# Kernel tuning notes

Hardware: AMD Instinct MI355X
Metric: run time of the kernel (lower is better)

Reference implementation:

```python
import jax, jax.numpy as jnp
import numpy as np

N_NODES = 100000
N_EDGES = 1000000
D_IN = 64
D_OUT = 64
K_HOPS = 3


def setup_inputs() -> dict:
    key = jax.random.key(0)
    k1, k2, k3 = jax.random.split(key, 3)
    x = jax.random.normal(k1, (N_NODES, D_IN), dtype=jnp.float32)
    edge_index = jax.random.randint(k2, (2, N_EDGES), 0, N_NODES, dtype=jnp.int64)
    # Linear layer params (PyG Linear: y = x @ W.T + b)
    W = jax.random.normal(k3, (D_OUT, D_IN), dtype=jnp.float32) * (1.0 / np.sqrt(D_IN))
    b = jnp.zeros((D_OUT,), dtype=jnp.float32)
    return {"x": x, "edge_index": edge_index, "W": W, "b": b}


def reference(x, edge_index, W, b):
    # SGConv: x' = (D^{-1/2} (A + I) D^{-1/2})^K x, then Linear.
    N = x.shape[0]
    src, dst = edge_index[0], edge_index[1]
    loop = jnp.arange(N, dtype=edge_index.dtype)
    src = jnp.concatenate([src, loop])  # add self loops
    dst = jnp.concatenate([dst, loop])
    ones = jnp.ones(src.shape[0], dtype=x.dtype)
    deg = jax.ops.segment_sum(ones, dst, num_segments=N)  # in-degree incl. self loop
    dinv = jnp.where(deg > 0, jax.lax.rsqrt(deg), jnp.zeros_like(deg))
    norm = dinv[src] * dinv[dst]  # [E+N]
    for _ in range(K_HOPS):
        # out[dst] += norm * x[src]
        x = jax.ops.segment_sum(norm[:, None] * x[src], dst, num_segments=N)
    return x @ W.T + b
```

## Files before the change

kernel.cpp:

```cpp
#include <hip/hip_runtime.h>

#define NN 100000
#define NE 1000000
#define D  64
#define CAP 32
#define OVF_CAP 16384

#define FILL_EPT 8
#define FILL_CHUNK (256 * FILL_EPT)
#define FILL_NCHUNK ((NE + FILL_CHUNK - 1) / FILL_CHUNK)
#define PART_SZ 12500

__device__ __forceinline__ unsigned bf16rne(float f) {
    unsigned h = __float_as_uint(f);
    return (h + 0x7fffu + ((h >> 16) & 1u)) >> 16;
}
__device__ __forceinline__ uint2 pack4(float4 v) {
    uint2 o;
    o.x = bf16rne(v.x) | (bf16rne(v.y) << 16);
    o.y = bf16rne(v.z) | (bf16rne(v.w) << 16);
    return o;
}
__device__ __forceinline__ float4 unpack4(uint2 u) {
    float4 f;
    f.x = __uint_as_float(u.x << 16);
    f.y = __uint_as_float(u.x & 0xffff0000u);
    f.z = __uint_as_float(u.y << 16);
    f.w = __uint_as_float(u.y & 0xffff0000u);
    return f;
}

__global__ __launch_bounds__(256) void k_fill_bucket(const int* __restrict__ src,
                                                     const int* __restrict__ dst,
                                                     int* __restrict__ cnt,
                                                     int* __restrict__ bucket,
                                                     int* __restrict__ ovf_n,
                                                     int2* __restrict__ ovf) {
    const int part = blockIdx.x & 7;
    const int lo = part * PART_SZ, hi = lo + PART_SZ;
    const int base = (blockIdx.x >> 3) * FILL_CHUNK + threadIdx.x;
    #pragma unroll
    for (int it = 0; it < FILL_EPT; ++it) {
        int e = base + it * 256;
        if (e < NE) {
            int d = __builtin_nontemporal_load(&dst[e]);
            if (d >= lo && d < hi) {
                int s = __builtin_nontemporal_load(&src[e]);
                int c = atomicAdd(&cnt[d], 1);
                if (c < CAP) {
                    bucket[(size_t)d * CAP + c] = s;
                } else {
                    int i = atomicAdd(ovf_n, 1);
                    if (i < OVF_CAP) ovf[i] = make_int2(s, d);
                }
            }
        }
    }
}

__global__ void k_cvt(const float2* __restrict__ x2, unsigned* __restrict__ xb,
                      const int* __restrict__ cnt, float* __restrict__ dinv) {
    int i = blockIdx.x * blockDim.x + threadIdx.x;
    unsigned long long v = __builtin_nontemporal_load((const unsigned long long*)&x2[i]);
    float vx = __uint_as_float((unsigned)(v & 0xffffffffu));
    float vy = __uint_as_float((unsigned)(v >> 32));
    xb[i] = bf16rne(vx) | (bf16rne(vy) << 16);
    if (i < NN) dinv[i] = rsqrtf((float)(cnt[i] + 1));
}


__global__ __launch_bounds__(256) void k_gather_bf16(const uint2* __restrict__ in2,
                                                     const int* __restrict__ cnt,
                                                     const int* __restrict__ bucket,
                                                     const float* __restrict__ dinv,
                                                     const int* __restrict__ ovf_n,
                                                     const int2* __restrict__ ovf,
                                                     uint2* __restrict__ out2) {
    const int tid = threadIdx.x;
    const int l = tid & 15;
    const int n = blockIdx.x * 16 + (tid >> 4);

    const int deg = min(cnt[n], CAP);
    const float dn = dinv[n];

    float4 a0 = unpack4(in2[(size_t)n * 16 + l]);
    a0.x *= dn; a0.y *= dn; a0.z *= dn; a0.w *= dn;
    float4 a1 = make_float4(0.f, 0.f, 0.f, 0.f);
    float4 a2 = make_float4(0.f, 0.f, 0.f, 0.f);
    float4 a3 = make_float4(0.f, 0.f, 0.f, 0.f);

    if (deg > 0) {
        int   iA = (l < deg) ? l : 0;
        int   sA = bucket[(size_t)n * CAP + iA];
        float wA = dinv[sA];
        const int kmax = deg < 16 ? deg : 16;
        int k = 0;
        for (; k + 3 < kmax; k += 4) {
            int   s0 = __shfl(sA, k + 0, 16);
            int   s1 = __shfl(sA, k + 1, 16);
            int   s2 = __shfl(sA, k + 2, 16);
            int   s3 = __shfl(sA, k + 3, 16);
            float w0 = __shfl(wA, k + 0, 16);
            float w1 = __shfl(wA, k + 1, 16);
            float w2 = __shfl(wA, k + 2, 16);
            float w3 = __shfl(wA, k + 3, 16);
            float4 r0 = unpack4(in2[(size_t)s0 * 16 + l]);
            float4 r1 = unpack4(in2[(size_t)s1 * 16 + l]);
            float4 r2 = unpack4(in2[(size_t)s2 * 16 + l]);
            float4 r3 = unpack4(in2[(size_t)s3 * 16 + l]);
            a0.x = fmaf(w0, r0.x, a0.x); a0.y = fmaf(w0, r0.y, a0.y);
            a0.z = fmaf(w0, r0.z, a0.z); a0.w = fmaf(w0, r0.w, a0.w);
            a1.x = fmaf(w1, r1.x, a1.x); a1.y = fmaf(w1, r1.y, a1.y);
            a1.z = fmaf(w1, r1.z, a1.z); a1.w = fmaf(w1, r1.w, a1.w);
            a2.x = fmaf(w2, r2.x, a2.x); a2.y = fmaf(w2, r2.y, a2.y);
            a2.z = fmaf(w2, r2.z, a2.z); a2.w = fmaf(w2, r2.w, a2.w);
            a3.x = fmaf(w3, r3.x, a3.x); a3.y = fmaf(w3, r3.y, a3.y);
            a3.z = fmaf(w3, r3.z, a3.z); a3.w = fmaf(w3, r3.w, a3.w);
        }
        for (; k < kmax; ++k) {
            int   s0 = __shfl(sA, k, 16);
            float w0 = __shfl(wA, k, 16);
            float4 r0 = unpack4(in2[(size_t)s0 * 16 + l]);
            a0.x = fmaf(w0, r0.x, a0.x); a0.y = fmaf(w0, r0.y, a0.y);
            a0.z = fmaf(w0, r0.z, a0.z); a0.w = fmaf(w0, r0.w, a0.w);
        }
        if (deg > 16) {
            int   iB = (16 + l < deg) ? (16 + l) : 0;
            int   sB = bucket[(size_t)n * CAP + iB];
            float wB = dinv[sB];
            const int k2max = deg - 16;
            int k2 = 0;
            for (; k2 + 1 < k2max; k2 += 2) {
                int   s0 = __shfl(sB, k2 + 0, 16);
                int   s1 = __shfl(sB, k2 + 1, 16);
                float w0 = __shfl(wB, k2 + 0, 16);
                float w1 = __shfl(wB, k2 + 1, 16);
                float4 r0 = unpack4(in2[(size_t)s0 * 16 + l]);
                float4 r1 = unpack4(in2[(size_t)s1 * 16 + l]);
                a1.x = fmaf(w0, r0.x, a1.x); a1.y = fmaf(w0, r0.y, a1.y);
                a1.z = fmaf(w0, r0.z, a1.z); a1.w = fmaf(w0, r0.w, a1.w);
                a2.x = fmaf(w1, r1.x, a2.x); a2.y = fmaf(w1, r1.y, a2.y);
                a2.z = fmaf(w1, r1.z, a2.z); a2.w = fmaf(w1, r1.w, a2.w);
            }
            if (k2 < k2max) {
                int   s0 = __shfl(sB, k2, 16);
                float w0 = __shfl(wB, k2, 16);
                float4 r0 = unpack4(in2[(size_t)s0 * 16 + l]);
                a3.x = fmaf(w0, r0.x, a3.x); a3.y = fmaf(w0, r0.y, a3.y);
                a3.z = fmaf(w0, r0.z, a3.z); a3.w = fmaf(w0, r0.w, a3.w);
            }
        }
    }

    int m = *ovf_n;
    if (m > 0) {
        if (m > OVF_CAP) m = OVF_CAP;
        for (int i = 0; i < m; ++i) {
            int2 p = ovf[i];
            if (p.y == n) {
                float w = dinv[p.x];
                float4 r = unpack4(in2[(size_t)p.x * 16 + l]);
                a0.x = fmaf(w, r.x, a0.x); a0.y = fmaf(w, r.y, a0.y);
                a0.z = fmaf(w, r.z, a0.z); a0.w = fmaf(w, r.w, a0.w);
            }
        }
    }

    float4 r;
    r.x = dn * ((a0.x + a1.x) + (a2.x + a3.x));
    r.y = dn * ((a0.y + a1.y) + (a2.y + a3.y));
    r.z = dn * ((a0.z + a1.z) + (a2.z + a3.z));
    r.w = dn * ((a0.w + a1.w) + (a2.w + a3.w));
    out2[(size_t)n * 16 + l] = pack4(r);
}

__global__ __launch_bounds__(256) void k_linear_reg(const unsigned short* __restrict__ inb,
                                                    const float* __restrict__ W,
                                                    const float* __restrict__ bias,
                                                    float* __restrict__ out) {
    const int lane = threadIdx.x & 63;
    const int wid  = (blockIdx.x * blockDim.x + threadIdx.x) >> 6;
    const int nw   = (gridDim.x * blockDim.x) >> 6;

    float w[64];
    const float4* W4 = (const float4*)W;
    #pragma unroll
    for (int i = 0; i < 16; ++i) {
        float4 q = W4[lane * 16 + i];
        w[4 * i + 0] = q.x; w[4 * i + 1] = q.y;
        w[4 * i + 2] = q.z; w[4 * i + 3] = q.w;
    }
    const float bo = bias[lane];

    for (int n = wid; n < NN; n += nw) {
        unsigned short rh = __builtin_nontemporal_load(&inb[(size_t)n * 64 + lane]);
        int rli = (int)((unsigned)rh << 16);
        float y0 = bo, y1 = 0.f;
        #pragma unroll
        for (int i = 0; i < 64; i += 2) {
            y0 = fmaf(__int_as_float(__builtin_amdgcn_readlane(rli, i)),     w[i],     y0);
            y1 = fmaf(__int_as_float(__builtin_amdgcn_readlane(rli, i + 1)), w[i + 1], y1);
        }
        __builtin_nontemporal_store(y0 + y1, &out[(size_t)n * 64 + lane]);
    }
}


__global__ void k_init_deg(float* __restrict__ deg) {
    int n = blockIdx.x * blockDim.x + threadIdx.x;
    if (n < NN) deg[n] = 1.0f;
}
__global__ void k_count_deg(const int* __restrict__ dst, float* __restrict__ deg) {
    int e = blockIdx.x * blockDim.x + threadIdx.x;
    if (e < NE) atomicAdd(&deg[dst[e]], 1.0f);
}
__global__ void k_dinv_f(float* __restrict__ deg) {
    int n = blockIdx.x * blockDim.x + threadIdx.x;
    if (n < NN) deg[n] = rsqrtf(deg[n]);
}
__global__ void k_prop_init(const float* __restrict__ in, const float* __restrict__ dinv,
                            float* __restrict__ out) {
    int i = blockIdx.x * blockDim.x + threadIdx.x;
    if (i < NN * D) {
        int n = i >> 6;
        float di = dinv[n];
        out[i] = di * di * in[i];
    }
}
__global__ __launch_bounds__(256) void k_prop_edges(const float* __restrict__ in,
                                                    const int* __restrict__ src,
                                                    const int* __restrict__ dst,
                                                    const float* __restrict__ dinv,
                                                    float* __restrict__ out) {
    int t = blockIdx.x * blockDim.x + threadIdx.x;
    int e = t >> 6, f = t & 63;
    if (e < NE) {
        int s = src[e], d = dst[e];
        float w = dinv[s] * dinv[d];
        atomicAdd(&out[d * D + f], w * in[s * D + f]);
    }
}
__global__ __launch_bounds__(256) void k_linear(const float* __restrict__ in,
                                                const float* __restrict__ W,
                                                const float* __restrict__ bias,
                                                float* __restrict__ out) {
    __shared__ float Wt[64 * 65];
    __shared__ float rows[4][64];
    const int tid = threadIdx.x;
    for (int m = tid; m < 64 * 64; m += 256) {
        int o = m >> 6, i = m & 63;
        Wt[i * 65 + o] = W[m];
    }
    __syncthreads();
    const int wave = tid >> 6, lane = tid & 63;
    const float bo = bias[lane];
    for (int base = blockIdx.x * 4; base < NN; base += gridDim.x * 4) {
        int n = base + wave;
        if (n < NN) {
            rows[wave][lane] = in[n * D + lane];
            float acc = bo;
            #pragma unroll
            for (int i = 0; i < 64; ++i)
                acc = fmaf(rows[wave][i], Wt[i * 65 + lane], acc);
            out[n * D + lane] = acc;
        }
    }
}


extern "C" void kernel_launch(void* const* d_in, const int* in_sizes, int n_in,
                              void* d_out, int out_size, void* d_ws, size_t ws_size,
                              hipStream_t stream) {
    const float* x   = (const float*)d_in[0];
    const int*   ei  = (const int*)d_in[1];
    const float* W   = (const float*)d_in[2];
    const float* b   = (const float*)d_in[3];
    float* out = (float*)d_out;

    const int* src = ei;
    const int* dst = ei + NE;

    char* ws = (char*)d_ws;
    size_t off = 0;
    auto take = [&](size_t bytes) -> char* {
        char* p = ws + off;
        off = (off + bytes + 255) & ~(size_t)255;
        return p;
    };

    int*      cnt    = (int*)take((size_t)NN * 4);
    float*    dinv   = (float*)take((size_t)NN * 4);
    int*      ovf_n  = (int*)take(256);
    int2*     ovf    = (int2*)take((size_t)OVF_CAP * 8);
    unsigned* P      = (unsigned*)take((size_t)NN * 32 * 4);
    unsigned* Q      = (unsigned*)take((size_t)NN * 32 * 4);
    int*      bucket = (int*)take((size_t)NN * CAP * 4);
    float*    buf    = (float*)P;
    const bool use_bucket = (off <= ws_size);

    const int B = 256;
    const int gridE1 = (NE + B - 1) / B;
    const int gridN1 = (NN + B - 1) / B;
    const int gridNW = NN / 16;

    if (use_bucket) {
        hipMemsetAsync(cnt, 0, (size_t)NN * 4, stream);
        hipMemsetAsync(ovf_n, 0, 4, stream);
        k_fill_bucket<<<FILL_NCHUNK * 8, B, 0, stream>>>(src, dst, cnt, bucket, ovf_n, ovf);
        k_cvt<<<12500, B, 0, stream>>>((const float2*)x, P, cnt, dinv);

        k_gather_bf16<<<gridNW, B, 0, stream>>>((const uint2*)P, cnt, bucket, dinv, ovf_n, ovf, (uint2*)Q);
        k_gather_bf16<<<gridNW, B, 0, stream>>>((const uint2*)Q, cnt, bucket, dinv, ovf_n, ovf, (uint2*)P);
        k_gather_bf16<<<gridNW, B, 0, stream>>>((const uint2*)P, cnt, bucket, dinv, ovf_n, ovf, (uint2*)Q);
        k_linear_reg<<<1024, B, 0, stream>>>((const unsigned short*)Q, W, b, out);
    } else {
        const int gridF = (NN * D + B - 1) / B;
        const int gridEW = (NE * 64) / B;
        k_init_deg <<<gridN1, B, 0, stream>>>(dinv);
        k_count_deg<<<gridE1, B, 0, stream>>>(dst, dinv);
        k_dinv_f   <<<gridN1, B, 0, stream>>>(dinv);
        k_prop_init <<<gridF, B, 0, stream>>>(x, dinv, buf);
        k_prop_edges<<<gridEW, B, 0, stream>>>(x, src, dst, dinv, buf);
        k_prop_init <<<gridF, B, 0, stream>>>(buf, dinv, out);
        k_prop_edges<<<gridEW, B, 0, stream>>>(buf, src, dst, dinv, out);
        k_prop_init <<<gridF, B, 0, stream>>>(out, dinv, buf);
        k_prop_edges<<<gridEW, B, 0, stream>>>(out, src, dst, dinv, buf);
        k_linear<<<NN / 4, B, 0, stream>>>(buf, W, b, out);
    }
}
```

Measured before the change: 173.7 us.

## Fold memsets into convert kernel, stage bucket fill via LDS, recompute dinv inline

Zeroing of the degree counters and overflow counter moves into the bf16 conversion kernel, which now runs before bucket fill, so the two memset launches go away. The separate dinv array is dropped and each gather recomputes rsqrt(cnt+1) from the counts. The fill kernel first collects its selected edges into a shared-memory list and only then does the global atomics. This trims launches and dinv traffic at the cost of extra cnt loads and rsqrt work in every gather pass, plus an extra barrier and LDS staging in the fill kernel.

```diff
diff --git a/kernel.cpp b/kernel.cpp
--- a/kernel.cpp
+++ b/kernel.cpp
@@ -10,6 +10,7 @@
 #define FILL_CHUNK (256 * FILL_EPT)
 #define FILL_NCHUNK ((NE + FILL_CHUNK - 1) / FILL_CHUNK)
 #define PART_SZ 12500
+#define SELCAP 512
 
 __device__ __forceinline__ unsigned bf16rne(float f) {
     unsigned h = __float_as_uint(f);
@@ -30,49 +31,63 @@
     return f;
 }
 
+__global__ void k_cvt(const float2* __restrict__ x2, unsigned* __restrict__ xb,
+                      int* __restrict__ cnt, int* __restrict__ ovf_n) {
+    int i = blockIdx.x * blockDim.x + threadIdx.x;
+    unsigned long long v = __builtin_nontemporal_load((const unsigned long long*)&x2[i]);
+    float vx = __uint_as_float((unsigned)(v & 0xffffffffu));
+    float vy = __uint_as_float((unsigned)(v >> 32));
+    xb[i] = bf16rne(vx) | (bf16rne(vy) << 16);
+    if (i < NN) cnt[i] = 0;
+    if (i == 0) *ovf_n = 0;
+}
+
 __global__ __launch_bounds__(256) void k_fill_bucket(const int* __restrict__ src,
                                                      const int* __restrict__ dst,
                                                      int* __restrict__ cnt,
                                                      int* __restrict__ bucket,
                                                      int* __restrict__ ovf_n,
                                                      int2* __restrict__ ovf) {
+    __shared__ int nsel;
+    __shared__ int2 sel[SELCAP];
     const int part = blockIdx.x & 7;
     const int lo = part * PART_SZ, hi = lo + PART_SZ;
     const int base = (blockIdx.x >> 3) * FILL_CHUNK + threadIdx.x;
+
+    if (threadIdx.x == 0) nsel = 0;
+    __syncthreads();
+
     #pragma unroll
     for (int it = 0; it < FILL_EPT; ++it) {
         int e = base + it * 256;
-        if (e < NE) {
-            int d = __builtin_nontemporal_load(&dst[e]);
-            if (d >= lo && d < hi) {
-                int s = __builtin_nontemporal_load(&src[e]);
+        int d = (e < NE) ? __builtin_nontemporal_load(&dst[e]) : -1;
+        if (d >= lo && d < hi) {
+            int s = __builtin_nontemporal_load(&src[e]);
+            int slot = atomicAdd(&nsel, 1);
+            if (slot < SELCAP) {
+                sel[slot] = make_int2(s, d);
+            } else {
                 int c = atomicAdd(&cnt[d], 1);
-                if (c < CAP) {
-                    bucket[(size_t)d * CAP + c] = s;
-                } else {
-                    int i = atomicAdd(ovf_n, 1);
-                    if (i < OVF_CAP) ovf[i] = make_int2(s, d);
-                }
+                if (c < CAP) bucket[(size_t)d * CAP + c] = s;
+                else { int i = atomicAdd(ovf_n, 1); if (i < OVF_CAP) ovf[i] = make_int2(s, d); }
             }
         }
     }
-}
-
-__global__ void k_cvt(const float2* __restrict__ x2, unsigned* __restrict__ xb,
-                      const int* __restrict__ cnt, float* __restrict__ dinv) {
-    int i = blockIdx.x * blockDim.x + threadIdx.x;
-    unsigned long long v = __builtin_nontemporal_load((const unsigned long long*)&x2[i]);
-    float vx = __uint_as_float((unsigned)(v & 0xffffffffu));
-    float vy = __uint_as_float((unsigned)(v >> 32));
-    xb[i] = bf16rne(vx) | (bf16rne(vy) << 16);
-    if (i < NN) dinv[i] = rsqrtf((float)(cnt[i] + 1));
+    __syncthreads();
+
+    int m = min(nsel, SELCAP);
+    for (int i = threadIdx.x; i < m; i += 256) {
+        int2 p = sel[i];
+        int c = atomicAdd(&cnt[p.y], 1);
+        if (c < CAP) bucket[(size_t)p.y * CAP + c] = p.x;
+        else { int j = atomicAdd(ovf_n, 1); if (j < OVF_CAP) ovf[j] = make_int2(p.x, p.y); }
+    }
 }
 
 
 __global__ __launch_bounds__(256) void k_gather_bf16(const uint2* __restrict__ in2,
                                                      const int* __restrict__ cnt,
                                                      const int* __restrict__ bucket,
-                                                     const float* __restrict__ dinv,
                                                      const int* __restrict__ ovf_n,
                                                      const int2* __restrict__ ovf,
                                                      uint2* __restrict__ out2) {
@@ -80,8 +95,9 @@
     const int l = tid & 15;
     const int n = blockIdx.x * 16 + (tid >> 4);
 
-    const int deg = min(cnt[n], CAP);
-    const float dn = dinv[n];
+    const int cn = cnt[n];
+    const int deg = min(cn, CAP);
+    const float dn = rsqrtf((float)(cn + 1));
 
     float4 a0 = unpack4(in2[(size_t)n * 16 + l]);
     a0.x *= dn; a0.y *= dn; a0.z *= dn; a0.w *= dn;
@@ -92,7 +108,7 @@
     if (deg > 0) {
         int   iA = (l < deg) ? l : 0;
         int   sA = bucket[(size_t)n * CAP + iA];
-        float wA = dinv[sA];
+        float wA = rsqrtf((float)(cnt[sA] + 1));
         const int kmax = deg < 16 ? deg : 16;
         int k = 0;
         for (; k + 3 < kmax; k += 4) {
@@ -127,7 +143,7 @@
         if (deg > 16) {
             int   iB = (16 + l < deg) ? (16 + l) : 0;
             int   sB = bucket[(size_t)n * CAP + iB];
-            float wB = dinv[sB];
+            float wB = rsqrtf((float)(cnt[sB] + 1));
             const int k2max = deg - 16;
             int k2 = 0;
             for (; k2 + 1 < k2max; k2 += 2) {
@@ -158,7 +174,7 @@
         for (int i = 0; i < m; ++i) {
             int2 p = ovf[i];
             if (p.y == n) {
-                float w = dinv[p.x];
+                float w = rsqrtf((float)(cnt[p.x] + 1));
                 float4 r = unpack4(in2[(size_t)p.x * 16 + l]);
                 a0.x = fmaf(w, r.x, a0.x); a0.y = fmaf(w, r.y, a0.y);
                 a0.z = fmaf(w, r.z, a0.z); a0.w = fmaf(w, r.w, a0.w);
@@ -304,14 +320,12 @@
     const int gridNW = NN / 16;
 
     if (use_bucket) {
-        hipMemsetAsync(cnt, 0, (size_t)NN * 4, stream);
-        hipMemsetAsync(ovf_n, 0, 4, stream);
+        k_cvt<<<12500, B, 0, stream>>>((const float2*)x, P, cnt, ovf_n);
         k_fill_bucket<<<FILL_NCHUNK * 8, B, 0, stream>>>(src, dst, cnt, bucket, ovf_n, ovf);
-        k_cvt<<<12500, B, 0, stream>>>((const float2*)x, P, cnt, dinv);
-
-        k_gather_bf16<<<gridNW, B, 0, stream>>>((const uint2*)P, cnt, bucket, dinv, ovf_n, ovf, (uint2*)Q);
-        k_gather_bf16<<<gridNW, B, 0, stream>>>((const uint2*)Q, cnt, bucket, dinv, ovf_n, ovf, (uint2*)P);
-        k_gather_bf16<<<gridNW, B, 0, stream>>>((const uint2*)P, cnt, bucket, dinv, ovf_n, ovf, (uint2*)Q);
+
+        k_gather_bf16<<<gridNW, B, 0, stream>>>((const uint2*)P, cnt, bucket, ovf_n, ovf, (uint2*)Q);
+        k_gather_bf16<<<gridNW, B, 0, stream>>>((const uint2*)Q, cnt, bucket, ovf_n, ovf, (uint2*)P);
+        k_gather_bf16<<<gridNW, B, 0, stream>>>((const uint2*)P, cnt, bucket, ovf_n, ovf, (uint2*)Q);
         k_linear_reg<<<1024, B, 0, stream>>>((const unsigned short*)Q, W, b, out);
     } else {
         const int gridF = (NN * D + B - 1) / B;
```

Result: slower. 179.9 us (+3.6%).

## Apply linear layer before propagation and fuse bias into final gather

Applied to the files above, without the earlier changes.

Because propagation is linear and commutes with the right-multiplication by W, the linear layer is now applied first, fused with the bf16 conversion, and the bias add is fused into the last gather, which writes fp32 output directly. This removes the separate linear kernel and its bf16 read plus fp32 write pass over the node features. The dinv array is no longer written; each gather recomputes rsqrt from the counts. The two memsets are merged into one. Rounding the features to bf16 after the matmul instead of before slightly changes numerics, and the extra cnt gathers per neighbor add scattered loads.

```diff
diff --git a/kernel.cpp b/kernel.cpp
--- a/kernel.cpp
+++ b/kernel.cpp
@@ -58,30 +58,52 @@
     }
 }
 
-__global__ void k_cvt(const float2* __restrict__ x2, unsigned* __restrict__ xb,
-                      const int* __restrict__ cnt, float* __restrict__ dinv) {
-    int i = blockIdx.x * blockDim.x + threadIdx.x;
-    unsigned long long v = __builtin_nontemporal_load((const unsigned long long*)&x2[i]);
-    float vx = __uint_as_float((unsigned)(v & 0xffffffffu));
-    float vy = __uint_as_float((unsigned)(v >> 32));
-    xb[i] = bf16rne(vx) | (bf16rne(vy) << 16);
-    if (i < NN) dinv[i] = rsqrtf((float)(cnt[i] + 1));
-}
-
-
-__global__ __launch_bounds__(256) void k_gather_bf16(const uint2* __restrict__ in2,
-                                                     const int* __restrict__ cnt,
-                                                     const int* __restrict__ bucket,
-                                                     const float* __restrict__ dinv,
-                                                     const int* __restrict__ ovf_n,
-                                                     const int2* __restrict__ ovf,
-                                                     uint2* __restrict__ out2) {
+__global__ __launch_bounds__(256) void k_cvt_linw(const float* __restrict__ x,
+                                                  const float* __restrict__ W,
+                                                  unsigned short* __restrict__ P) {
+    const int lane = threadIdx.x & 63;
+    const int wid  = (blockIdx.x * blockDim.x + threadIdx.x) >> 6;
+    const int nw   = (gridDim.x * blockDim.x) >> 6;
+
+    float w[64];
+    const float4* W4 = (const float4*)W;
+    #pragma unroll
+    for (int i = 0; i < 16; ++i) {
+        float4 q = W4[lane * 16 + i];
+        w[4 * i + 0] = q.x; w[4 * i + 1] = q.y;
+        w[4 * i + 2] = q.z; w[4 * i + 3] = q.w;
+    }
+
+    for (int n = wid; n < NN; n += nw) {
+        float xl = __builtin_nontemporal_load(&x[(size_t)n * 64 + lane]);
+        int xi = __float_as_int(xl);
+        float y0 = 0.f, y1 = 0.f;
+        #pragma unroll
+        for (int i = 0; i < 64; i += 2) {
+            y0 = fmaf(__int_as_float(__builtin_amdgcn_readlane(xi, i)),     w[i],     y0);
+            y1 = fmaf(__int_as_float(__builtin_amdgcn_readlane(xi, i + 1)), w[i + 1], y1);
+        }
+        P[(size_t)n * 64 + lane] = (unsigned short)bf16rne(y0 + y1);
+    }
+}
+
+
+template <bool F32OUT>
+__device__ __forceinline__ void gather_body(const uint2* __restrict__ in2,
+                                            const int* __restrict__ cnt,
+                                            const int* __restrict__ bucket,
+                                            const int* __restrict__ ovf_n,
+                                            const int2* __restrict__ ovf,
+                                            const float* __restrict__ bias,
+                                            uint2* __restrict__ out2,
+                                            float4* __restrict__ out4) {
     const int tid = threadIdx.x;
     const int l = tid & 15;
     const int n = blockIdx.x * 16 + (tid >> 4);
 
-    const int deg = min(cnt[n], CAP);
-    const float dn = dinv[n];
+    const int cn = cnt[n];
+    const int deg = min(cn, CAP);
+    const float dn = rsqrtf((float)(cn + 1));
 
     float4 a0 = unpack4(in2[(size_t)n * 16 + l]);
     a0.x *= dn; a0.y *= dn; a0.z *= dn; a0.w *= dn;
@@ -92,7 +114,7 @@
     if (deg > 0) {
         int   iA = (l < deg) ? l : 0;
         int   sA = bucket[(size_t)n * CAP + iA];
-        float wA = dinv[sA];
+        float wA = rsqrtf((float)(cnt[sA] + 1));
         const int kmax = deg < 16 ? deg : 16;
         int k = 0;
         for (; k + 3 < kmax; k += 4) {
@@ -127,7 +149,7 @@
         if (deg > 16) {
             int   iB = (16 + l < deg) ? (16 + l) : 0;
             int   sB = bucket[(size_t)n * CAP + iB];
-            float wB = dinv[sB];
+            float wB = rsqrtf((float)(cnt[sB] + 1));
             const int k2max = deg - 16;
             int k2 = 0;
             for (; k2 + 1 < k2max; k2 += 2) {
@@ -158,7 +180,7 @@
         for (int i = 0; i < m; ++i) {
             int2 p = ovf[i];
             if (p.y == n) {
-                float w = dinv[p.x];
+                float w = rsqrtf((float)(cnt[p.x] + 1));
                 float4 r = unpack4(in2[(size_t)p.x * 16 + l]);
                 a0.x = fmaf(w, r.x, a0.x); a0.y = fmaf(w, r.y, a0.y);
                 a0.z = fmaf(w, r.z, a0.z); a0.w = fmaf(w, r.w, a0.w);
@@ -171,38 +193,32 @@
     r.y = dn * ((a0.y + a1.y) + (a2.y + a3.y));
     r.z = dn * ((a0.z + a1.z) + (a2.z + a3.z));
     r.w = dn * ((a0.w + a1.w) + (a2.w + a3.w));
-    out2[(size_t)n * 16 + l] = pack4(r);
-}
-
-__global__ __launch_bounds__(256) void k_linear_reg(const unsigned short* __restrict__ inb,
-                                                    const float* __restrict__ W,
+    if (F32OUT) {
+        float4 bv = *(const float4*)&bias[4 * l];
+        r.x += bv.x; r.y += bv.y; r.z += bv.z; r.w += bv.w;
+        out4[(size_t)n * 16 + l] = r;
+    } else {
+        out2[(size_t)n * 16 + l] = pack4(r);
+    }
+}
+
+__global__ __launch_bounds__(256) void k_gather_bf16(const uint2* __restrict__ in2,
+                                                     const int* __restrict__ cnt,
+                                                     const int* __restrict__ bucket,
+                                                     const int* __restrict__ ovf_n,
+                                                     const int2* __restrict__ ovf,
+                                                     uint2* __restrict__ out2) {
+    gather_body<false>(in2, cnt, bucket, ovf_n, ovf, nullptr, out2, nullptr);
+}
+
+__global__ __launch_bounds__(256) void k_gather_out(const uint2* __restrict__ in2,
+                                                    const int* __restrict__ cnt,
+                                                    const int* __restrict__ bucket,
+                                                    const int* __restrict__ ovf_n,
+                                                    const int2* __restrict__ ovf,
                                                     const float* __restrict__ bias,
-                                                    float* __restrict__ out) {
-    const int lane = threadIdx.x & 63;
-    const int wid  = (blockIdx.x * blockDim.x + threadIdx.x) >> 6;
-    const int nw   = (gridDim.x * blockDim.x) >> 6;
-
-    float w[64];
-    const float4* W4 = (const float4*)W;
-    #pragma unroll
-    for (int i = 0; i < 16; ++i) {
-        float4 q = W4[lane * 16 + i];
-        w[4 * i + 0] = q.x; w[4 * i + 1] = q.y;
-        w[4 * i + 2] = q.z; w[4 * i + 3] = q.w;
-    }
-    const float bo = bias[lane];
-
-    for (int n = wid; n < NN; n += nw) {
-        unsigned short rh = __builtin_nontemporal_load(&inb[(size_t)n * 64 + lane]);
-        int rli = (int)((unsigned)rh << 16);
-        float y0 = bo, y1 = 0.f;
-        #pragma unroll
-        for (int i = 0; i < 64; i += 2) {
-            y0 = fmaf(__int_as_float(__builtin_amdgcn_readlane(rli, i)),     w[i],     y0);
-            y1 = fmaf(__int_as_float(__builtin_amdgcn_readlane(rli, i + 1)), w[i + 1], y1);
-        }
-        __builtin_nontemporal_store(y0 + y1, &out[(size_t)n * 64 + lane]);
-    }
+                                                    float4* __restrict__ out4) {
+    gather_body<true>(in2, cnt, bucket, ovf_n, ovf, bias, nullptr, out4);
 }
 
 
@@ -288,14 +304,14 @@
         return p;
     };
 
-    int*      cnt    = (int*)take((size_t)NN * 4);
-    float*    dinv   = (float*)take((size_t)NN * 4);
-    int*      ovf_n  = (int*)take(256);
-    int2*     ovf    = (int2*)take((size_t)OVF_CAP * 8);
-    unsigned* P      = (unsigned*)take((size_t)NN * 32 * 4);
-    unsigned* Q      = (unsigned*)take((size_t)NN * 32 * 4);
-    int*      bucket = (int*)take((size_t)NN * CAP * 4);
-    float*    buf    = (float*)P;
+    int*            cnt    = (int*)take((size_t)NN * 4);
+    int*            ovf_n  = (int*)take(256);
+    float*          dinv   = (float*)take((size_t)NN * 4);
+    int2*           ovf    = (int2*)take((size_t)OVF_CAP * 8);
+    unsigned short* P      = (unsigned short*)take((size_t)NN * 64 * 2);
+    unsigned short* Q      = (unsigned short*)take((size_t)NN * 64 * 2);
+    int*            bucket = (int*)take((size_t)NN * CAP * 4);
+    float*          buf    = (float*)P;
     const bool use_bucket = (off <= ws_size);
 
     const int B = 256;
@@ -304,15 +320,13 @@
     const int gridNW = NN / 16;
 
     if (use_bucket) {
-        hipMemsetAsync(cnt, 0, (size_t)NN * 4, stream);
-        hipMemsetAsync(ovf_n, 0, 4, stream);
+        size_t zlen = (size_t)((char*)ovf_n - (char*)cnt) + 256;
+        (void)hipMemsetAsync(cnt, 0, zlen, stream);
         k_fill_bucket<<<FILL_NCHUNK * 8, B, 0, stream>>>(src, dst, cnt, bucket, ovf_n, ovf);
-        k_cvt<<<12500, B, 0, stream>>>((const float2*)x, P, cnt, dinv);
-
-        k_gather_bf16<<<gridNW, B, 0, stream>>>((const uint2*)P, cnt, bucket, dinv, ovf_n, ovf, (uint2*)Q);
-        k_gather_bf16<<<gridNW, B, 0, stream>>>((const uint2*)Q, cnt, bucket, dinv, ovf_n, ovf, (uint2*)P);
-        k_gather_bf16<<<gridNW, B, 0, stream>>>((const uint2*)P, cnt, bucket, dinv, ovf_n, ovf, (uint2*)Q);
-        k_linear_reg<<<1024, B, 0, stream>>>((const unsigned short*)Q, W, b, out);
+        k_cvt_linw<<<2048, B, 0, stream>>>(x, W, P);
+        k_gather_bf16<<<gridNW, B, 0, stream>>>((const uint2*)P, cnt, bucket, ovf_n, ovf, (uint2*)Q);
+        k_gather_bf16<<<gridNW, B, 0, stream>>>((const uint2*)Q, cnt, bucket, ovf_n, ovf, (uint2*)P);
+        k_gather_out<<<gridNW, B, 0, stream>>>((const uint2*)P, cnt, bucket, ovf_n, ovf, b, (float4*)out);
     } else {
         const int gridF = (NN * D + B - 1) / B;
         const int gridEW = (NE * 64) / B;
```

New measurement: 172.0 us. About the same (-1.0%).
